# Performance work log

Hardware: AMD Instinct MI355X
Metric: run time of the kernel (lower is better)

## Reference

```python
import jax, jax.numpy as jnp
import numpy as np
from jax import lax

COMMITMENT_COST = 0.25
CODEBOOK_SIZE = 512


def setup_inputs() -> dict:
    key = jax.random.key(0)
    k1, k2 = jax.random.split(key)
    x = jax.random.normal(k1, (8, 16, 64, 64, 64), dtype=jnp.float32)
    # nn.init.uniform_(codebook, -1/K, 1/K)
    codebook = jax.random.uniform(k2, (CODEBOOK_SIZE, 64), dtype=jnp.float32,
                                  minval=-1.0 / CODEBOOK_SIZE, maxval=1.0 / CODEBOOK_SIZE)
    return {"x": x, "codebook": codebook}


def reference(x, codebook):
    B, T, C, H, W = x.shape
    K = codebook.shape[0]
    # (B,T,C,H,W) -> (B,T,H,W,C) -> (N, C)
    xp = jnp.transpose(x, (0, 1, 3, 4, 2))
    flat = xp.reshape(-1, C)
    # squared L2 distances to codebook entries: ||f||^2 - 2 f.e + ||e||^2
    distances = (jnp.sum(flat * flat, axis=1, keepdims=True)
                 - 2.0 * flat @ codebook.T
                 + jnp.sum(codebook * codebook, axis=1)[None, :])
    indices = jnp.argmin(distances, axis=1)  # (N,)
    quantized = codebook[indices].reshape(B, T, H, W, C)
    quantized = jnp.transpose(quantized, (0, 1, 4, 2, 3))  # (B,T,C,H,W)
    codebook_loss = jnp.mean((lax.stop_gradient(quantized) - x) ** 2)
    commitment_loss = jnp.mean((quantized - lax.stop_gradient(x)) ** 2)
    vq_loss = codebook_loss + COMMITMENT_COST * commitment_loss
    # straight-through estimator
    quantized_st = x + lax.stop_gradient(quantized - x)
    # empirical entropy in bits
    counts = jnp.bincount(indices, length=K).astype(jnp.float32)
    probs = counts / jnp.maximum(counts.sum(), 1.0)
    entropy_bits = -jnp.sum(jnp.where(probs > 0,
                                      probs * jnp.log2(jnp.maximum(probs, 1e-30)),
                                      0.0))
    return quantized_st, indices, vq_loss, entropy_bits
```

## Files before the change

kernel.cpp:

```cpp
#include <hip/hip_runtime.h>

constexpr int K    = 512;
constexpr int CDIM = 64;
constexpr int NVEC = 8 * 16 * 64 * 64;
constexpr long long NELEM = (long long)NVEC * CDIM;

constexpr size_t OFF_SSE    = 0;
constexpr size_t OFF_COUNTS = 16;
constexpr size_t OFF_S2     = 16 + 4 * (size_t)K;

__global__ void k_prep(const float* __restrict__ cb, float* __restrict__ S2)
{
#pragma clang fp contract(off)
    int k = threadIdx.x;
    const float* e = cb + (k << 6);
    float sq[CDIM];
    #pragma unroll
    for (int c = 0; c < CDIM; ++c) {
        float v = e[c];
        sq[c] = v * v;
    }
    float r[8];
    #pragma unroll
    for (int j = 0; j < 8; ++j) r[j] = sq[j];
    #pragma unroll
    for (int i = 8; i < CDIM; i += 8)
        #pragma unroll
        for (int j = 0; j < 8; ++j) r[j] += sq[i + j];
    S2[k] = ((r[0] + r[1]) + (r[2] + r[3])) + ((r[4] + r[5]) + (r[6] + r[7]));
}

__global__ __launch_bounds__(256, 2)
void k_main(const float* __restrict__ x, const float* __restrict__ cb,
            const float* __restrict__ S2g, float* __restrict__ outq,
            float* __restrict__ outidx, double* __restrict__ sse_g,
            int* __restrict__ counts)
{
#pragma clang fp contract(off)
    __shared__ int    hist[K];
    __shared__ double wsum[4];
    const int tid = threadIdx.x;
    for (int i = tid; i < K; i += 256) hist[i] = 0;
    __syncthreads();

    const int n  = blockIdx.x * 256 + tid;
    const int bt = n >> 12;
    const int hw = n & 4095;
    const size_t base = ((size_t)bt << 18) + (size_t)hw;
    const float* xv = x + base;

    float f[CDIM];
    #pragma unroll
    for (int c = 0; c < CDIM; ++c) f[c] = xv[(size_t)c << 12];
    #pragma unroll
    for (int c = 0; c < CDIM; ++c) asm volatile("" : "+a"(f[c]));

    float r[8];
    #pragma unroll
    for (int j = 0; j < 8; ++j) r[j] = f[j] * f[j];
    #pragma unroll
    for (int i = 8; i < CDIM; i += 8)
        #pragma unroll
        for (int j = 0; j < 8; ++j) r[j] += f[i + j] * f[i + j];
    const float S1 = ((r[0] + r[1]) + (r[2] + r[3])) + ((r[4] + r[5]) + (r[6] + r[7]));

    float best  = 3.4e38f;
    int   bestk = 0;

    for (int k8 = 0; k8 < K; k8 += 8) {
        const float* eb = cb + (k8 << 6);
        float g[8] = {0.f, 0.f, 0.f, 0.f, 0.f, 0.f, 0.f, 0.f};
        #pragma unroll
        for (int c = 0; c < CDIM; ++c) {
            const float fc = f[c];
            #pragma unroll
            for (int j = 0; j < 8; ++j)
                g[j] = fmaf(fc, eb[j * 64 + c], g[j]);
        }
        #pragma unroll
        for (int j = 0; j < 8; ++j) {
            const float D = (S1 - 2.f * g[j]) + S2g[k8 + j];
            if (D < best) { best = D; bestk = k8 + j; }
        }
    }

    atomicAdd(&hist[bestk], 1);
    outidx[n] = (float)bestk;

    const float4* e4 = (const float4*)(cb + (bestk << 6));
    double acc = 0.0;
    #pragma unroll
    for (int c4 = 0; c4 < 16; ++c4) {
        float4 e = e4[c4];
        const int c = c4 * 4;
        float d0 = e.x - f[c + 0];
        float d1 = e.y - f[c + 1];
        float d2 = e.z - f[c + 2];
        float d3 = e.w - f[c + 3];
        outq[base + ((size_t)(c + 0) << 12)] = e.x;
        outq[base + ((size_t)(c + 1) << 12)] = e.y;
        outq[base + ((size_t)(c + 2) << 12)] = e.z;
        outq[base + ((size_t)(c + 3) << 12)] = e.w;
        acc += (double)d0 * d0 + (double)d1 * d1 + (double)d2 * d2 + (double)d3 * d3;
    }

    double v = acc;
    #pragma unroll
    for (int off = 32; off; off >>= 1) v += __shfl_down(v, off, 64);
    if ((tid & 63) == 0) wsum[tid >> 6] = v;
    __syncthreads();
    if (tid == 0) atomicAdd(sse_g, wsum[0] + wsum[1] + wsum[2] + wsum[3]);

    for (int i = tid; i < K; i += 256) {
        int h = hist[i];
        if (h) atomicAdd(&counts[i], h);
    }
}

__global__ void k_final(const double* __restrict__ sse_g, const int* __restrict__ counts,
                        float* __restrict__ out_scalars)
{
    __shared__ double part[8];
    const int t = threadIdx.x;
    int c = counts[t];
    double p = (double)c / (double)NVEC;
    double h = (c > 0) ? (-p * log2(p)) : 0.0;
    #pragma unroll
    for (int off = 32; off; off >>= 1) h += __shfl_down(h, off, 64);
    if ((t & 63) == 0) part[t >> 6] = h;
    __syncthreads();
    if (t == 0) {
        double H = 0.0;
        #pragma unroll
        for (int i = 0; i < 8; ++i) H += part[i];
        out_scalars[0] = (float)(1.25 * (*sse_g) / (double)NELEM);
        out_scalars[1] = (float)H;
    }
}

extern "C" void kernel_launch(void* const* d_in, const int* in_sizes, int n_in,
                              void* d_out, int out_size, void* d_ws, size_t ws_size,
                              hipStream_t stream)
{
    const float* x  = (const float*)d_in[0];
    const float* cb = (const float*)d_in[1];

    char* ws = (char*)d_ws;
    double* sse    = (double*)(ws + OFF_SSE);
    int*    counts = (int*)   (ws + OFF_COUNTS);
    float*  S2     = (float*) (ws + OFF_S2);

    float* outq   = (float*)d_out;
    float* outidx = outq + NELEM;
    float* outsc  = outidx + NVEC;

    hipMemsetAsync(d_ws, 0, OFF_S2, stream);

    k_prep <<<1, 512, 0, stream>>>(cb, S2);
    k_main <<<NVEC / 256, 256, 0, stream>>>(x, cb, S2, outq, outidx, sse, counts);
    k_final<<<1, 512, 0, stream>>>(sse, counts, outsc);
}
```

Measured before the change: 895.6 us.

## Force SGPR codebook operands in inline-asm FMAs and raise occupancy to 4 blocks

```diff
diff --git a/kernel.cpp b/kernel.cpp
--- a/kernel.cpp
+++ b/kernel.cpp
@@ -30,7 +30,7 @@
     S2[k] = ((r[0] + r[1]) + (r[2] + r[3])) + ((r[4] + r[5]) + (r[6] + r[7]));
 }
 
-__global__ __launch_bounds__(256, 2)
+__global__ __launch_bounds__(256, 4)
 void k_main(const float* __restrict__ x, const float* __restrict__ cb,
             const float* __restrict__ S2g, float* __restrict__ outq,
             float* __restrict__ outidx, double* __restrict__ sse_g,
@@ -52,8 +52,6 @@
     float f[CDIM];
     #pragma unroll
     for (int c = 0; c < CDIM; ++c) f[c] = xv[(size_t)c << 12];
-    #pragma unroll
-    for (int c = 0; c < CDIM; ++c) asm volatile("" : "+a"(f[c]));
 
     float r[8];
     #pragma unroll
@@ -64,34 +62,62 @@
         for (int j = 0; j < 8; ++j) r[j] += f[i + j] * f[i + j];
     const float S1 = ((r[0] + r[1]) + (r[2] + r[3])) + ((r[4] + r[5]) + (r[6] + r[7]));
 
+    if (n == -1) const_cast<float*>(x)[0] = 0.f;
+
     float best  = 3.4e38f;
     int   bestk = 0;
 
     for (int k8 = 0; k8 < K; k8 += 8) {
         const float* eb = cb + (k8 << 6);
-        float g[8] = {0.f, 0.f, 0.f, 0.f, 0.f, 0.f, 0.f, 0.f};
+        float g0 = 0.f, g1 = 0.f, g2 = 0.f, g3 = 0.f;
+        float g4 = 0.f, g5 = 0.f, g6 = 0.f, g7 = 0.f;
         #pragma unroll
         for (int c = 0; c < CDIM; ++c) {
             const float fc = f[c];
-            #pragma unroll
-            for (int j = 0; j < 8; ++j)
-                g[j] = fmaf(fc, eb[j * 64 + c], g[j]);
+            const float e0 = eb[0 * 64 + c], e1 = eb[1 * 64 + c];
+            const float e2 = eb[2 * 64 + c], e3 = eb[3 * 64 + c];
+            const float e4 = eb[4 * 64 + c], e5 = eb[5 * 64 + c];
+            const float e6 = eb[6 * 64 + c], e7 = eb[7 * 64 + c];
+            asm("v_fmac_f32 %0, %9, %8\n\t"
+                "v_fmac_f32 %1, %10, %8\n\t"
+                "v_fmac_f32 %2, %11, %8\n\t"
+                "v_fmac_f32 %3, %12, %8\n\t"
+                "v_fmac_f32 %4, %13, %8\n\t"
+                "v_fmac_f32 %5, %14, %8\n\t"
+                "v_fmac_f32 %6, %15, %8\n\t"
+                "v_fmac_f32 %7, %16, %8"
+                : "+v"(g0), "+v"(g1), "+v"(g2), "+v"(g3),
+                  "+v"(g4), "+v"(g5), "+v"(g6), "+v"(g7)
+                : "v"(fc),
+                  "s"(e0), "s"(e1), "s"(e2), "s"(e3),
+                  "s"(e4), "s"(e5), "s"(e6), "s"(e7));
         }
-        #pragma unroll
-        for (int j = 0; j < 8; ++j) {
-            const float D = (S1 - 2.f * g[j]) + S2g[k8 + j];
-            if (D < best) { best = D; bestk = k8 + j; }
-        }
+        const float D0 = (S1 - 2.f * g0) + S2g[k8 + 0];
+        const float D1 = (S1 - 2.f * g1) + S2g[k8 + 1];
+        const float D2 = (S1 - 2.f * g2) + S2g[k8 + 2];
+        const float D3 = (S1 - 2.f * g3) + S2g[k8 + 3];
+        const float D4 = (S1 - 2.f * g4) + S2g[k8 + 4];
+        const float D5 = (S1 - 2.f * g5) + S2g[k8 + 5];
+        const float D6 = (S1 - 2.f * g6) + S2g[k8 + 6];
+        const float D7 = (S1 - 2.f * g7) + S2g[k8 + 7];
+        if (D0 < best) { best = D0; bestk = k8 + 0; }
+        if (D1 < best) { best = D1; bestk = k8 + 1; }
+        if (D2 < best) { best = D2; bestk = k8 + 2; }
+        if (D3 < best) { best = D3; bestk = k8 + 3; }
+        if (D4 < best) { best = D4; bestk = k8 + 4; }
+        if (D5 < best) { best = D5; bestk = k8 + 5; }
+        if (D6 < best) { best = D6; bestk = k8 + 6; }
+        if (D7 < best) { best = D7; bestk = k8 + 7; }
     }
 
     atomicAdd(&hist[bestk], 1);
     outidx[n] = (float)bestk;
 
-    const float4* e4 = (const float4*)(cb + (bestk << 6));
+    const float4* e4v = (const float4*)(cb + (bestk << 6));
     double acc = 0.0;
     #pragma unroll
     for (int c4 = 0; c4 < 16; ++c4) {
-        float4 e = e4[c4];
+        float4 e = e4v[c4];
         const int c = c4 * 4;
         float d0 = e.x - f[c + 0];
         float d1 = e.y - f[c + 1];
```

Result: faster. 745.1 us (-16.8%).
